# Performance work log

Hardware: AMD Instinct MI355X
Metric: run time of the kernel (lower is better)

## Reference

```python
import jax, jax.numpy as jnp
import numpy as np

B, T, D = 512, 256, 64
LATENT = 128
H = 2 * LATENT  # hidden size = latent_dim * 2


def setup_inputs() -> dict:
    key = jax.random.key(0)
    ks = jax.random.split(key, 16)
    x = jax.random.normal(ks[0], (B, T, D), dtype=jnp.float32)
    # strictly increasing time points
    tps = jnp.cumsum(jax.random.uniform(ks[1], (T,), dtype=jnp.float32, minval=0.01, maxval=0.1))
    # ragged mask: each trajectory observed for a random prefix length in [1, T]
    lengths = jax.random.randint(ks[2], (B,), 1, T + 1)
    mask = (jnp.arange(T)[None, :] < lengths[:, None]).astype(jnp.float32)
    s = 0.05
    # GRUCell params (torch layout: gates ordered r, z, n)
    w_ih = jax.random.normal(ks[3], (3 * H, D), dtype=jnp.float32) * s
    w_hh = jax.random.normal(ks[4], (3 * H, H), dtype=jnp.float32) * s
    b_ih = jax.random.normal(ks[5], (3 * H,), dtype=jnp.float32) * s
    b_hh = jax.random.normal(ks[6], (3 * H,), dtype=jnp.float32) * s
    # Neural ODE func: Linear -> tanh -> Linear
    w1 = jax.random.normal(ks[7], (H, H), dtype=jnp.float32) * s
    b1 = jax.random.normal(ks[8], (H,), dtype=jnp.float32) * s
    w2 = jax.random.normal(ks[9], (H, H), dtype=jnp.float32) * s
    b2 = jax.random.normal(ks[10], (H,), dtype=jnp.float32) * s
    # output linear
    w_out = jax.random.normal(ks[11], (H, H), dtype=jnp.float32) * s
    b_out = jax.random.normal(ks[12], (H,), dtype=jnp.float32) * s
    return {"x": x, "tps": tps, "mask": mask, "w_ih": w_ih, "w_hh": w_hh,
            "b_ih": b_ih, "b_hh": b_hh, "w1": w1, "b1": b1, "w2": w2,
            "b2": b2, "w_out": w_out, "b_out": b_out}


def _gru_ode_forward(x, tps, mask, w_ih, w_hh, b_ih, b_hh, w1, b1, w2, b2, w_out, b_out):
    Bn, Tn, _ = x.shape
    # right_fill_mask: 1 wherever some earlier timestep (strictly before j) was observed
    r_fill = ((jnp.cumsum(mask, axis=1) - mask) > 0).astype(x.dtype)  # (B,T)
    # Euler dt per step; dt[0] is unused (r_fill[:,0]==0 forces h_ode=h at i=0)
    dt = jnp.diff(tps, prepend=tps[:1] - 0.01)  # (T,)

    def node_f(h):
        return jnp.tanh(h @ w1.T + b1) @ w2.T + b2

    def gru_cell(x_t, h):
        gi = x_t @ w_ih.T + b_ih
        gh = h @ w_hh.T + b_hh
        gi_r, gi_z, gi_n = jnp.split(gi, 3, axis=-1)
        gh_r, gh_z, gh_n = jnp.split(gh, 3, axis=-1)
        r = jax.nn.sigmoid(gi_r + gh_r)
        z = jax.nn.sigmoid(gi_z + gh_z)
        n = jnp.tanh(gi_n + r * gh_n)
        return (1.0 - z) * n + z * h

    def step(h, inp):
        x_t, dt_t, m_t, r_t = inp  # (B,D), (), (B,), (B,)
        h_euler = h + dt_t * node_f(h)          # single Euler step
        r_c = r_t[:, None]
        h_ode = h_euler * r_c + h * (1.0 - r_c)  # freeze state before first obs
        h_rnn = gru_cell(x_t, h_ode)
        m_c = m_t[:, None]
        h_new = h_rnn * m_c + h_ode * (1.0 - m_c)  # update only at observations
        return h_new, h_new

    h0 = jnp.zeros((Bn, H), dtype=x.dtype)
    xs = (jnp.swapaxes(x, 0, 1), dt, mask.T, r_fill.T)
    _, h_arr = jax.lax.scan(step, h0, xs)  # (T,B,H)
    # last observed timestep per trajectory
    ind = (Tn - 1) - jnp.argmax(mask[:, ::-1], axis=1)  # (B,)
    h_last = h_arr[ind, jnp.arange(Bn)]  # (B,H)
    return h_last @ w_out.T + b_out


def reference(x, tps, mask, w_ih, w_hh, b_ih, b_hh, w1, b1, w2, b2, w_out, b_out):
    return _gru_ode_forward(x, tps, mask, w_ih, w_hh, b_ih, b_hh, w1, b1, w2, b2, w_out, b_out)
```

## Files before the change

kernel.cpp:

```cpp
#include <hip/hip_runtime.h>
#include <hip/hip_bf16.h>


#define Bn 512
#define Tn 256
#define Dn 64
#define Hn 256

typedef __bf16 bf16x8 __attribute__((ext_vector_type(8)));
typedef float f32x4 __attribute__((ext_vector_type(4)));

__device__ __forceinline__ f32x4 mfma_bf16(bf16x8 a, bf16x8 b, f32x4 c) {
  return __builtin_amdgcn_mfma_f32_16x16x32_bf16(a, b, c, 0, 0, 0);
}
__device__ __forceinline__ float fast_sigmoid(float x) {
  return __builtin_amdgcn_rcpf(1.0f + __expf(-x));
}
__device__ __forceinline__ float fast_tanh(float x) {
  return 1.0f - 2.0f * __builtin_amdgcn_rcpf(1.0f + __expf(2.0f * x));
}

__global__ void pack_w(const float* __restrict__ w, __bf16* __restrict__ out,
                       int N, int K) {
  int idx = blockIdx.x * blockDim.x + threadIdx.x;
  if (idx >= N * K) return;
  int n = idx / K, k = idx % K;
  int tile = n >> 4, kb = k >> 5;
  int lane = (n & 15) + (((k & 31) >> 3) << 4);
  int j = k & 7;
  out[(((tile * (K >> 5) + kb) << 6) + lane) * 8 + j] = (__bf16)w[idx];
}

__global__ void pack_w_hilo(const float* __restrict__ w, __bf16* __restrict__ hi,
                            __bf16* __restrict__ lo, int N, int K) {
  int idx = blockIdx.x * blockDim.x + threadIdx.x;
  if (idx >= N * K) return;
  int n = idx / K, k = idx % K;
  int tile = n >> 4, kb = k >> 5;
  int lane = (n & 15) + (((k & 31) >> 3) << 4);
  int j = k & 7;
  int o = (((tile * (K >> 5) + kb) << 6) + lane) * 8 + j;
  float f = w[idx];
  __bf16 h = (__bf16)f;
  hi[o] = h;
  lo[o] = (__bf16)(f - (float)h);
}

#define BAR()                                        \
  asm volatile("s_waitcnt lgkmcnt(0)" ::: "memory"); \
  __builtin_amdgcn_sched_barrier(0);                 \
  __builtin_amdgcn_s_barrier();                      \
  __builtin_amdgcn_sched_barrier(0);

#define CHUNK_Q(p) (((p) >= 6) ? (p) - 6 : (p))
#define CHUNK_TILE(p) (((CHUNK_Q(p) >> 1) << 4) + 2 * wv + (CHUNK_Q(p) & 1))
#define CHUNK_KB0(p) (((p) >= 6) ? 4 : 0)
#define ISSUE_CHUNK(p, b)                                                  \
  {                                                                        \
    const int tl_ = CHUNK_TILE(p), kb_ = CHUNK_KB0(p);                     \
    _Pragma("unroll") for (int f_ = 0; f_ < 4; f_++)                       \
        wb[b][f_] = whf[(tl_ * 8 + kb_ + f_) * 64 + l];                    \
  }

__launch_bounds__(512, 2)
__global__ void gru_ode_kernel(
    const float* __restrict__ x, const float* __restrict__ tps,
    const float* __restrict__ mask,
    const float* __restrict__ b_ih, const float* __restrict__ b_hh,
    const float* __restrict__ b1, const float* __restrict__ b2,
    const float* __restrict__ b_out,
    const __bf16* __restrict__ w1p, const __bf16* __restrict__ w2p,
    const __bf16* __restrict__ whhp, const __bf16* __restrict__ wihp,
    const __bf16* __restrict__ wouth, const __bf16* __restrict__ woutl,
    float* __restrict__ out) {
  __shared__ __align__(16) __bf16 wih_l[49152];
  __shared__ __align__(16) __bf16 h_fr[4096];
  __shared__ __align__(16) __bf16 a_fr[4096];
  __shared__ __align__(16) __bf16 o_fr[4096];
  __shared__ __align__(16) float hlast[16][260];
  __shared__ float dt_s[Tn];
  __shared__ int len_s[16];
  __shared__ int maxlen_s;

  const int tid = threadIdx.x;
  const int wv = tid >> 6;
  const int l = tid & 63;
  const int g = l >> 4;
  const int c = l & 15;
  const int m0 = blockIdx.x << 4;

  if (tid < Tn) dt_s[tid] = tid ? tps[tid] - tps[tid - 1] : 0.01f;
#pragma unroll
  for (int i = 0; i < 8; i++) o_fr[tid + i * 512] = (__bf16)0.0f;
  {
    const int4* s4 = (const int4*)wihp;
    int4* d4 = (int4*)wih_l;
    for (int i = tid; i < 6144; i += 512) d4[i] = s4[i];
  }
  {
    int m = tid >> 5, l32 = tid & 31;
    const float* mr = mask + (size_t)(m0 + m) * Tn + l32 * 8;
    float s = 0.f;
#pragma unroll
    for (int i = 0; i < 8; i++) s += mr[i];
#pragma unroll
    for (int o = 16; o; o >>= 1) s += __shfl_down(s, o, 32);
    if (l32 == 0) len_s[m] = (int)(s + 0.5f);
  }
  __syncthreads();
  if (tid == 0) {
    int mx = 1;
    for (int i = 0; i < 16; i++) mx = max(mx, len_s[i]);
    maxlen_s = mx;
  }
  __syncthreads();
  const int maxlen = maxlen_s;
  int len4[4];
#pragma unroll
  for (int r = 0; r < 4; r++) len4[r] = len_s[4 * g + r];

  float bb1[2], bb2[2], brz[4], bin[2], bhn[2], bo[2];
#pragma unroll
  for (int nt = 0; nt < 2; nt++) {
    int col = 32 * wv + 16 * nt + c;
    bb1[nt] = b1[col];
    bb2[nt] = b2[col];
    brz[nt] = b_ih[col] + b_hh[col];
    brz[2 + nt] = b_ih[256 + col] + b_hh[256 + col];
    bin[nt] = b_ih[512 + col];
    bhn[nt] = b_hh[512 + col];
    bo[nt] = b_out[col];
  }

  bf16x8 w1f[2][8], w2f[2][8];
#pragma unroll
  for (int nt = 0; nt < 2; nt++)
#pragma unroll
    for (int kb = 0; kb < 8; kb++) {
      w1f[nt][kb] = *(const bf16x8*)&w1p[(((2 * wv + nt) * 8 + kb) * 64 + l) * 8];
      w2f[nt][kb] = *(const bf16x8*)&w2p[(((2 * wv + nt) * 8 + kb) * 64 + l) * 8];
    }

  float hreg[2][4] = {{0, 0, 0, 0}, {0, 0, 0, 0}};

  const bf16x8* whf = (const bf16x8*)whhp;
  const bf16x8* wifl = (const bf16x8*)wih_l;
  const float* xrow = x + (size_t)(m0 + c) * (Tn * Dn) + 8 * g;

  const int wbase = (wv * 64 + 4 * g + 16 * (c >> 3)) * 8 + (c & 7);

  for (int t = 0; t < maxlen; t++) {
    const float* xp = xrow + t * Dn;
    f32x4 xr0 = *(const f32x4*)(xp);
    f32x4 xr1 = *(const f32x4*)(xp + 4);
    f32x4 xr2 = *(const f32x4*)(xp + 32);
    f32x4 xr3 = *(const f32x4*)(xp + 36);
    bf16x8 wb[2][4];
    ISSUE_CHUNK(0, 0);
    ISSUE_CHUNK(1, 1);

    if (t > 0) {
      {
        bf16x8 hfv[8];
#pragma unroll
        for (int kb = 0; kb < 8; kb++)
          hfv[kb] = *(const bf16x8*)&h_fr[(kb * 64 + l) * 8];
#pragma unroll
        for (int nt = 0; nt < 2; nt++) {
          f32x4 acc = {0.f, 0.f, 0.f, 0.f};
#pragma unroll
          for (int kb = 0; kb < 8; kb++) acc = mfma_bf16(hfv[kb], w1f[nt][kb], acc);
#pragma unroll
          for (int r = 0; r < 4; r++)
            a_fr[wbase + (r + 32 * nt) * 8] = (__bf16)fast_tanh(acc[r] + bb1[nt]);
        }
      }
      BAR();
      {
        const float dtv = dt_s[t];
        bf16x8 afv[8];
#pragma unroll
        for (int kb = 0; kb < 8; kb++)
          afv[kb] = *(const bf16x8*)&a_fr[(kb * 64 + l) * 8];
#pragma unroll
        for (int nt = 0; nt < 2; nt++) {
          f32x4 acc = {0.f, 0.f, 0.f, 0.f};
#pragma unroll
          for (int kb = 0; kb < 8; kb++) acc = mfma_bf16(afv[kb], w2f[nt][kb], acc);
#pragma unroll
          for (int r = 0; r < 4; r++) {
            hreg[nt][r] += dtv * (acc[r] + bb2[nt]);
            o_fr[wbase + (r + 32 * nt) * 8] = (__bf16)hreg[nt][r];
          }
        }
      }
      BAR();
    }

    bf16x8 xf0, xf1;
#pragma unroll
    for (int j = 0; j < 4; j++) {
      xf0[j] = (__bf16)xr0[j];
      xf0[4 + j] = (__bf16)xr1[j];
      xf1[j] = (__bf16)xr2[j];
      xf1[4 + j] = (__bf16)xr3[j];
    }
    f32x4 acc6[6], agi2[2];
#pragma unroll
    for (int q = 0; q < 6; q++) acc6[q] = (f32x4){0.f, 0.f, 0.f, 0.f};
    agi2[0] = (f32x4){0.f, 0.f, 0.f, 0.f};
    agi2[1] = (f32x4){0.f, 0.f, 0.f, 0.f};

    bf16x8 ofv[4];
#pragma unroll
    for (int p = 0; p < 12; p++) {
      const int kb0 = CHUNK_KB0(p);
      const int q = CHUNK_Q(p);
      const int gate = q >> 1, nt = q & 1;
      if (p == 0 || p == 6) {
#pragma unroll
        for (int f = 0; f < 4; f++)
          ofv[f] = *(const bf16x8*)&o_fr[((kb0 + f) * 64 + l) * 8];
      }
      f32x4& accr = (gate == 0) ? acc6[nt] : (gate == 1) ? acc6[2 + nt] : acc6[4 + nt];
#pragma unroll
      for (int f = 0; f < 4; f++) accr = mfma_bf16(ofv[f], wb[p & 1][f], accr);
      if (p < 10) {
        ISSUE_CHUNK(p + 2, p & 1);
      }
    }
#pragma unroll
    for (int gg = 0; gg < 3; gg++) {
#pragma unroll
      for (int f = 0; f < 4; f++) {
        const int tile = gg * 16 + 2 * wv + (f >> 1);
        bf16x8 wf = wifl[(tile * 2 + (f & 1)) * 64 + l];
        if (gg < 2)
          acc6[gg * 2 + (f >> 1)] = mfma_bf16((f & 1) ? xf1 : xf0, wf, acc6[gg * 2 + (f >> 1)]);
        else
          agi2[f >> 1] = mfma_bf16((f & 1) ? xf1 : xf0, wf, agi2[f >> 1]);
      }
    }

#pragma unroll
    for (int nt = 0; nt < 2; nt++) {
#pragma unroll
      for (int r = 0; r < 4; r++) {
        float rg = fast_sigmoid(acc6[nt][r] + brz[nt]);
        float zg = fast_sigmoid(acc6[2 + nt][r] + brz[2 + nt]);
        float ng = fast_tanh(agi2[nt][r] + bin[nt] + rg * (acc6[4 + nt][r] + bhn[nt]));
        float hn = (1.f - zg) * ng + zg * hreg[nt][r];
        hreg[nt][r] = hn;
        if (t == len4[r] - 1) hlast[4 * g + r][32 * wv + 16 * nt + c] = hn;
        h_fr[wbase + (r + 32 * nt) * 8] = (__bf16)hn;
      }
    }
    BAR();
  }

  const bf16x8* woh = (const bf16x8*)wouth;
  const bf16x8* wol = (const bf16x8*)woutl;
  f32x4 oa[2] = {{0.f, 0.f, 0.f, 0.f}, {0.f, 0.f, 0.f, 0.f}};
#pragma unroll
  for (int kb = 0; kb < 8; kb++) {
    f32x4 v0 = *(const f32x4*)&hlast[c][kb * 32 + 8 * g];
    f32x4 v1 = *(const f32x4*)&hlast[c][kb * 32 + 8 * g + 4];
    bf16x8 hhi, hlo;
#pragma unroll
    for (int j = 0; j < 4; j++) {
      __bf16 p = (__bf16)v0[j]; hhi[j] = p; hlo[j] = (__bf16)(v0[j] - (float)p);
      __bf16 q = (__bf16)v1[j]; hhi[4 + j] = q; hlo[4 + j] = (__bf16)(v1[j] - (float)q);
    }
#pragma unroll
    for (int nt = 0; nt < 2; nt++) {
      int tile = 2 * wv + nt;
      oa[nt] = mfma_bf16(hhi, woh[(tile * 8 + kb) * 64 + l], oa[nt]);
      oa[nt] = mfma_bf16(hlo, woh[(tile * 8 + kb) * 64 + l], oa[nt]);
      oa[nt] = mfma_bf16(hhi, wol[(tile * 8 + kb) * 64 + l], oa[nt]);
    }
  }
#pragma unroll
  for (int nt = 0; nt < 2; nt++)
#pragma unroll
    for (int r = 0; r < 4; r++)
      out[(size_t)(m0 + 4 * g + r) * Hn + 32 * wv + 16 * nt + c] = oa[nt][r] + bo[nt];
}

extern "C" void kernel_launch(void* const* d_in, const int* in_sizes, int n_in,
                              void* d_out, int out_size, void* d_ws, size_t ws_size,
                              hipStream_t stream) {
  const float* x = (const float*)d_in[0];
  const float* tps = (const float*)d_in[1];
  const float* mask = (const float*)d_in[2];
  const float* w_ih = (const float*)d_in[3];
  const float* w_hh = (const float*)d_in[4];
  const float* b_ih = (const float*)d_in[5];
  const float* b_hh = (const float*)d_in[6];
  const float* w1 = (const float*)d_in[7];
  const float* b1 = (const float*)d_in[8];
  const float* w2 = (const float*)d_in[9];
  const float* b2 = (const float*)d_in[10];
  const float* w_out = (const float*)d_in[11];
  const float* b_out = (const float*)d_in[12];

  char* ws = (char*)d_ws;
  __bf16* w1p = (__bf16*)(ws + 0);
  __bf16* w2p = (__bf16*)(ws + 131072);
  __bf16* whhp = (__bf16*)(ws + 262144);
  __bf16* wihp = (__bf16*)(ws + 655360);
  __bf16* wouth = (__bf16*)(ws + 753664);
  __bf16* woutl = (__bf16*)(ws + 884736);

  pack_w<<<(256 * 256 + 255) / 256, 256, 0, stream>>>(w1, w1p, 256, 256);
  pack_w<<<(256 * 256 + 255) / 256, 256, 0, stream>>>(w2, w2p, 256, 256);
  pack_w<<<(768 * 256 + 255) / 256, 256, 0, stream>>>(w_hh, whhp, 768, 256);
  pack_w<<<(768 * 64 + 255) / 256, 256, 0, stream>>>(w_ih, wihp, 768, 64);
  pack_w_hilo<<<(256 * 256 + 255) / 256, 256, 0, stream>>>(w_out, wouth, woutl, 256, 256);

  gru_ode_kernel<<<32, 512, 0, stream>>>(x, tps, mask, b_ih, b_hh, b1, b2, b_out,
                                         w1p, w2p, whhp, wihp, wouth, woutl,
                                         (float*)d_out);
}
```

Measured before the change: 2.723 ms.

## Stream W1/W2/Whh weights through a rotating 7-slot register ring buffer

```diff
diff --git a/kernel.cpp b/kernel.cpp
--- a/kernel.cpp
+++ b/kernel.cpp
@@ -19,6 +19,8 @@
 __device__ __forceinline__ float fast_tanh(float x) {
   return 1.0f - 2.0f * __builtin_amdgcn_rcpf(1.0f + __expf(2.0f * x));
 }
+__device__ __forceinline__ bf16x8 as_bf16x8(int4 v) { return __builtin_bit_cast(bf16x8, v); }
+__device__ __forceinline__ f32x4 as_f32x4(int4 v) { return __builtin_bit_cast(f32x4, v); }
 
 __global__ void pack_w(const float* __restrict__ w, __bf16* __restrict__ out,
                        int N, int K) {
@@ -52,15 +54,23 @@
   __builtin_amdgcn_s_barrier();                      \
   __builtin_amdgcn_sched_barrier(0);
 
-#define CHUNK_Q(p) (((p) >= 6) ? (p) - 6 : (p))
-#define CHUNK_TILE(p) (((CHUNK_Q(p) >> 1) << 4) + 2 * wv + (CHUNK_Q(p) & 1))
-#define CHUNK_KB0(p) (((p) >= 6) ? 4 : 0)
-#define ISSUE_CHUNK(p, b)                                                  \
-  {                                                                        \
-    const int tl_ = CHUNK_TILE(p), kb_ = CHUNK_KB0(p);                     \
+#define LD_W1(B, i)                                                        \
+  { _Pragma("unroll") for (int f_ = 0; f_ < 4; f_++)                       \
+      wb[B][f_] = w1i[((2 * wv + ((i) >> 1)) * 8 + ((i) & 1) * 4 + f_) * 64 + l]; }
+#define LD_W2(B, i)                                                        \
+  { _Pragma("unroll") for (int f_ = 0; f_ < 4; f_++)                       \
+      wb[B][f_] = w2i[((2 * wv + ((i) >> 1)) * 8 + ((i) & 1) * 4 + f_) * 64 + l]; }
+#define LD_WH(B, j)                                                        \
+  { const int tl_ = (((j) % 6) >> 1) * 16 + 2 * wv + (((j) % 6) & 1);      \
+    const int k0_ = ((j) / 6) * 4;                                         \
     _Pragma("unroll") for (int f_ = 0; f_ < 4; f_++)                       \
-        wb[b][f_] = whf[(tl_ * 8 + kb_ + f_) * 64 + l];                    \
-  }
+        wb[B][f_] = whi[(tl_ * 8 + k0_ + f_) * 64 + l]; }
+#define LD_X(B, tt)                                                        \
+  { const float* xs_ = xrow + (((tt) < Tn) ? (tt) : Tn - 1) * Dn;          \
+    wb[B][0] = *(const int4*)(xs_);                                        \
+    wb[B][1] = *(const int4*)(xs_ + 4);                                    \
+    wb[B][2] = *(const int4*)(xs_ + 32);                                   \
+    wb[B][3] = *(const int4*)(xs_ + 36); }
 
 __launch_bounds__(512, 2)
 __global__ void gru_ode_kernel(
@@ -89,9 +99,12 @@
   const int c = l & 15;
   const int m0 = blockIdx.x << 4;
 
-  if (tid < Tn) dt_s[tid] = tid ? tps[tid] - tps[tid - 1] : 0.01f;
-#pragma unroll
-  for (int i = 0; i < 8; i++) o_fr[tid + i * 512] = (__bf16)0.0f;
+  if (tid < Tn) dt_s[tid] = tid ? tps[tid] - tps[tid - 1] : 0.0f;
+#pragma unroll
+  for (int i = 0; i < 8; i++) {
+    h_fr[tid + i * 512] = (__bf16)0.0f;
+    o_fr[tid + i * 512] = (__bf16)0.0f;
+  }
   {
     const int4* s4 = (const int4*)wihp;
     int4* d4 = (int4*)wih_l;
@@ -132,102 +145,138 @@
     bo[nt] = b_out[col];
   }
 
-  bf16x8 w1f[2][8], w2f[2][8];
-#pragma unroll
-  for (int nt = 0; nt < 2; nt++)
-#pragma unroll
-    for (int kb = 0; kb < 8; kb++) {
-      w1f[nt][kb] = *(const bf16x8*)&w1p[(((2 * wv + nt) * 8 + kb) * 64 + l) * 8];
-      w2f[nt][kb] = *(const bf16x8*)&w2p[(((2 * wv + nt) * 8 + kb) * 64 + l) * 8];
-    }
-
   float hreg[2][4] = {{0, 0, 0, 0}, {0, 0, 0, 0}};
 
-  const bf16x8* whf = (const bf16x8*)whhp;
+  const int4* w1i = (const int4*)w1p;
+  const int4* w2i = (const int4*)w2p;
+  const int4* whi = (const int4*)whhp;
   const bf16x8* wifl = (const bf16x8*)wih_l;
   const float* xrow = x + (size_t)(m0 + c) * (Tn * Dn) + 8 * g;
 
   const int wbase = (wv * 64 + 4 * g + 16 * (c >> 3)) * 8 + (c & 7);
 
+  int4 wb[7][4];
+  LD_X(0, 0);
+  LD_W1(1, 0);
+  LD_W1(2, 1);
+  LD_W1(3, 2);
+  LD_W1(4, 3);
+  LD_W2(5, 0);
+  LD_W2(6, 1);
+
   for (int t = 0; t < maxlen; t++) {
-    const float* xp = xrow + t * Dn;
-    f32x4 xr0 = *(const f32x4*)(xp);
-    f32x4 xr1 = *(const f32x4*)(xp + 4);
-    f32x4 xr2 = *(const f32x4*)(xp + 32);
-    f32x4 xr3 = *(const f32x4*)(xp + 36);
-    bf16x8 wb[2][4];
-    ISSUE_CHUNK(0, 0);
-    ISSUE_CHUNK(1, 1);
-
-    if (t > 0) {
-      {
-        bf16x8 hfv[8];
-#pragma unroll
-        for (int kb = 0; kb < 8; kb++)
-          hfv[kb] = *(const bf16x8*)&h_fr[(kb * 64 + l) * 8];
-#pragma unroll
-        for (int nt = 0; nt < 2; nt++) {
-          f32x4 acc = {0.f, 0.f, 0.f, 0.f};
-#pragma unroll
-          for (int kb = 0; kb < 8; kb++) acc = mfma_bf16(hfv[kb], w1f[nt][kb], acc);
-#pragma unroll
-          for (int r = 0; r < 4; r++)
-            a_fr[wbase + (r + 32 * nt) * 8] = (__bf16)fast_tanh(acc[r] + bb1[nt]);
-        }
-      }
-      BAR();
-      {
-        const float dtv = dt_s[t];
-        bf16x8 afv[8];
-#pragma unroll
-        for (int kb = 0; kb < 8; kb++)
-          afv[kb] = *(const bf16x8*)&a_fr[(kb * 64 + l) * 8];
-#pragma unroll
-        for (int nt = 0; nt < 2; nt++) {
-          f32x4 acc = {0.f, 0.f, 0.f, 0.f};
-#pragma unroll
-          for (int kb = 0; kb < 8; kb++) acc = mfma_bf16(afv[kb], w2f[nt][kb], acc);
-#pragma unroll
-          for (int r = 0; r < 4; r++) {
-            hreg[nt][r] += dtv * (acc[r] + bb2[nt]);
-            o_fr[wbase + (r + 32 * nt) * 8] = (__bf16)hreg[nt][r];
-          }
-        }
-      }
-      BAR();
-    }
-
     bf16x8 xf0, xf1;
-#pragma unroll
-    for (int j = 0; j < 4; j++) {
-      xf0[j] = (__bf16)xr0[j];
-      xf0[4 + j] = (__bf16)xr1[j];
-      xf1[j] = (__bf16)xr2[j];
-      xf1[4 + j] = (__bf16)xr3[j];
-    }
+    {
+      f32x4 a0 = as_f32x4(wb[0][0]), a1 = as_f32x4(wb[0][1]);
+      f32x4 a2 = as_f32x4(wb[0][2]), a3 = as_f32x4(wb[0][3]);
+#pragma unroll
+      for (int j = 0; j < 4; j++) {
+        xf0[j] = (__bf16)a0[j]; xf0[4 + j] = (__bf16)a1[j];
+        xf1[j] = (__bf16)a2[j]; xf1[4 + j] = (__bf16)a3[j];
+      }
+    }
+    LD_W2(0, 2);
+
+    {
+      bf16x8 hv[8];
+#pragma unroll
+      for (int kb = 0; kb < 8; kb++) hv[kb] = *(const bf16x8*)&h_fr[(kb * 64 + l) * 8];
+      f32x4 accA0 = {0.f, 0.f, 0.f, 0.f}, accA1 = {0.f, 0.f, 0.f, 0.f};
+#pragma unroll
+      for (int f = 0; f < 4; f++) accA0 = mfma_bf16(hv[f], as_bf16x8(wb[1][f]), accA0);
+      LD_W2(1, 3);
+#pragma unroll
+      for (int f = 0; f < 4; f++) accA0 = mfma_bf16(hv[4 + f], as_bf16x8(wb[2][f]), accA0);
+      LD_WH(2, 0);
+#pragma unroll
+      for (int f = 0; f < 4; f++) accA1 = mfma_bf16(hv[f], as_bf16x8(wb[3][f]), accA1);
+      LD_WH(3, 1);
+#pragma unroll
+      for (int f = 0; f < 4; f++) accA1 = mfma_bf16(hv[4 + f], as_bf16x8(wb[4][f]), accA1);
+      LD_WH(4, 2);
+#pragma unroll
+      for (int r = 0; r < 4; r++) {
+        a_fr[wbase + r * 8] = (__bf16)fast_tanh(accA0[r] + bb1[0]);
+        a_fr[wbase + (r + 32) * 8] = (__bf16)fast_tanh(accA1[r] + bb1[1]);
+      }
+    }
+    BAR();
+
+    {
+      bf16x8 av[8];
+#pragma unroll
+      for (int kb = 0; kb < 8; kb++) av[kb] = *(const bf16x8*)&a_fr[(kb * 64 + l) * 8];
+      f32x4 accB0 = {0.f, 0.f, 0.f, 0.f}, accB1 = {0.f, 0.f, 0.f, 0.f};
+#pragma unroll
+      for (int f = 0; f < 4; f++) accB0 = mfma_bf16(av[f], as_bf16x8(wb[5][f]), accB0);
+      LD_WH(5, 3);
+#pragma unroll
+      for (int f = 0; f < 4; f++) accB0 = mfma_bf16(av[4 + f], as_bf16x8(wb[6][f]), accB0);
+      LD_WH(6, 4);
+#pragma unroll
+      for (int f = 0; f < 4; f++) accB1 = mfma_bf16(av[f], as_bf16x8(wb[0][f]), accB1);
+      LD_WH(0, 5);
+#pragma unroll
+      for (int f = 0; f < 4; f++) accB1 = mfma_bf16(av[4 + f], as_bf16x8(wb[1][f]), accB1);
+      LD_WH(1, 6);
+      const float dtv = dt_s[t];
+#pragma unroll
+      for (int r = 0; r < 4; r++) {
+        hreg[0][r] += dtv * (accB0[r] + bb2[0]);
+        o_fr[wbase + r * 8] = (__bf16)hreg[0][r];
+        hreg[1][r] += dtv * (accB1[r] + bb2[1]);
+        o_fr[wbase + (r + 32) * 8] = (__bf16)hreg[1][r];
+      }
+    }
+    BAR();
+
     f32x4 acc6[6], agi2[2];
 #pragma unroll
     for (int q = 0; q < 6; q++) acc6[q] = (f32x4){0.f, 0.f, 0.f, 0.f};
     agi2[0] = (f32x4){0.f, 0.f, 0.f, 0.f};
     agi2[1] = (f32x4){0.f, 0.f, 0.f, 0.f};
-
-    bf16x8 ofv[4];
-#pragma unroll
-    for (int p = 0; p < 12; p++) {
-      const int kb0 = CHUNK_KB0(p);
-      const int q = CHUNK_Q(p);
-      const int gate = q >> 1, nt = q & 1;
-      if (p == 0 || p == 6) {
-#pragma unroll
-        for (int f = 0; f < 4; f++)
-          ofv[f] = *(const bf16x8*)&o_fr[((kb0 + f) * 64 + l) * 8];
-      }
-      f32x4& accr = (gate == 0) ? acc6[nt] : (gate == 1) ? acc6[2 + nt] : acc6[4 + nt];
-#pragma unroll
-      for (int f = 0; f < 4; f++) accr = mfma_bf16(ofv[f], wb[p & 1][f], accr);
-      if (p < 10) {
-        ISSUE_CHUNK(p + 2, p & 1);
-      }
+    {
+      bf16x8 ofv[4];
+#pragma unroll
+      for (int f = 0; f < 4; f++) ofv[f] = *(const bf16x8*)&o_fr[(f * 64 + l) * 8];
+#pragma unroll
+      for (int f = 0; f < 4; f++) acc6[0] = mfma_bf16(ofv[f], as_bf16x8(wb[2][f]), acc6[0]);
+      LD_WH(2, 7);
+#pragma unroll
+      for (int f = 0; f < 4; f++) acc6[1] = mfma_bf16(ofv[f], as_bf16x8(wb[3][f]), acc6[1]);
+      LD_WH(3, 8);
+#pragma unroll
+      for (int f = 0; f < 4; f++) acc6[2] = mfma_bf16(ofv[f], as_bf16x8(wb[4][f]), acc6[2]);
+      LD_WH(4, 9);
+#pragma unroll
+      for (int f = 0; f < 4; f++) acc6[3] = mfma_bf16(ofv[f], as_bf16x8(wb[5][f]), acc6[3]);
+      LD_WH(5, 10);
+#pragma unroll
+      for (int f = 0; f < 4; f++) acc6[4] = mfma_bf16(ofv[f], as_bf16x8(wb[6][f]), acc6[4]);
+      LD_WH(6, 11);
+#pragma unroll
+      for (int f = 0; f < 4; f++) acc6[5] = mfma_bf16(ofv[f], as_bf16x8(wb[0][f]), acc6[5]);
+      LD_X(0, t + 1);
+#pragma unroll
+      for (int f = 0; f < 4; f++) ofv[f] = *(const bf16x8*)&o_fr[((4 + f) * 64 + l) * 8];
+#pragma unroll
+      for (int f = 0; f < 4; f++) acc6[0] = mfma_bf16(ofv[f], as_bf16x8(wb[1][f]), acc6[0]);
+      LD_W1(1, 0);
+#pragma unroll
+      for (int f = 0; f < 4; f++) acc6[1] = mfma_bf16(ofv[f], as_bf16x8(wb[2][f]), acc6[1]);
+      LD_W1(2, 1);
+#pragma unroll
+      for (int f = 0; f < 4; f++) acc6[2] = mfma_bf16(ofv[f], as_bf16x8(wb[3][f]), acc6[2]);
+      LD_W1(3, 2);
+#pragma unroll
+      for (int f = 0; f < 4; f++) acc6[3] = mfma_bf16(ofv[f], as_bf16x8(wb[4][f]), acc6[3]);
+      LD_W1(4, 3);
+#pragma unroll
+      for (int f = 0; f < 4; f++) acc6[4] = mfma_bf16(ofv[f], as_bf16x8(wb[5][f]), acc6[4]);
+      LD_W2(5, 0);
+#pragma unroll
+      for (int f = 0; f < 4; f++) acc6[5] = mfma_bf16(ofv[f], as_bf16x8(wb[6][f]), acc6[5]);
+      LD_W2(6, 1);
     }
 #pragma unroll
     for (int gg = 0; gg < 3; gg++) {
```

Result: slower. 3.298 ms (+21.1%).
